# Performance work log

Measured on AMD Instinct MI355X. Metric: run time of the kernel, lower is better.

Reference implementation:

```python
import jax, jax.numpy as jnp
import numpy as np

ALPHA = 0.0005
TAU = 0.2


def setup_inputs() -> dict:
    key = jax.random.key(0)
    k1, k2, k3 = jax.random.split(key, 3)
    output = jax.random.normal(k1, (8192, 1000), dtype=jnp.float32)
    target = jax.random.normal(k2, (8192, 1000), dtype=jnp.float32)
    conv_w = jax.random.normal(k3, (256, 256, 128, 3), dtype=jnp.float32)
    return {"output": output, "target": target, "conv_w": conv_w}


def reference(output, target, conv_w):
    # base loss (nn.MSELoss with default 'mean' reduction)
    loss = jnp.mean((output - target) ** 2)

    # Diversity regularizer: pairwise cosine similarity between slices
    # conv_w[:, :, i, :] along dim 2 ('filters' = size(2) in the original).
    F = conv_w.shape[2]
    # V: [F, D] with D = out_ch * in_ch * kw
    V = jnp.transpose(conv_w, (2, 0, 1, 3)).reshape(F, -1)
    norms = jnp.linalg.norm(V, axis=1)                      # [F]
    G = (V @ V.T) / (norms[:, None] * norms[None, :])       # [F, F] cosine Gram

    # keep entries with tau < sim <= 1 and i != j
    offdiag = ~jnp.eye(F, dtype=bool)
    mask = (G > TAU) & (G <= 1.0) & offdiag
    reg = jnp.sum(jnp.where(mask, G, jnp.zeros((), dtype=G.dtype)))

    return loss + ALPHA * reg
```

## Files before the change

### kernel.cpp

```cpp
#include <hip/hip_runtime.h>
#include <hip/hip_bf16.h>


typedef __attribute__((ext_vector_type(8))) short bf16x8;
typedef __attribute__((ext_vector_type(4))) float f32x4;

#define ALPHA 0.0005f
#define TAU 0.2f

#define FDIM 128
#define NGRAM 1024
#define NMSE 2048
#define BLK_FLOATS 24576
#define NPAIRQ 8192
#define GRAM_ELEMS 16384
#define MSE_N4 2048000

__device__ __forceinline__ unsigned int pack_bf2(float lo, float hi) {
    union { float f; unsigned int u; } a, b;
    a.f = lo; b.f = hi;
    unsigned int al = (a.u + 0x7fffu + ((a.u >> 16) & 1u)) >> 16;
    unsigned int bh = (b.u + 0x7fffu + ((b.u >> 16) & 1u)) & 0xffff0000u;
    return (al & 0xffffu) | bh;
}

__device__ __forceinline__ uint4 make_frag(const float3& a, const float3& b) {
    uint4 r;
    r.x = pack_bf2(a.x, a.y);
    r.y = pack_bf2(a.z, b.x);
    r.z = pack_bf2(b.y, b.z);
    r.w = 0;
    return r;
}

__device__ __forceinline__ void load4(const float* __restrict__ p00,
                                      const float* __restrict__ p10,
                                      int c, float3 (&L)[4]) {
    const int co = c * 3072;
    L[0] = *reinterpret_cast<const float3*>(p00 + co);
    L[1] = *reinterpret_cast<const float3*>(p00 + co + 384);
    L[2] = *reinterpret_cast<const float3*>(p10 + co);
    L[3] = *reinterpret_cast<const float3*>(p10 + co + 384);
    __builtin_amdgcn_sched_barrier(0);
}

__device__ __forceinline__ void gram_chunk(
        const float* __restrict__ p00, const float* __restrict__ p10,
        int pre_c, bool dopre, float3 (&buf)[4],
        uint4 (*fragbuf)[64], int wave, int lane,
        f32x4 (&acc0)[8], f32x4 (&acc1)[8]) {
    const uint4 fA0 = make_frag(buf[0], buf[1]);
    const uint4 fA1 = make_frag(buf[2], buf[3]);
    if (dopre) load4(p00, p10, pre_c, buf);
    asm volatile("s_waitcnt lgkmcnt(0)" ::: "memory");
    __builtin_amdgcn_sched_barrier(0);
    __builtin_amdgcn_s_barrier();
    __builtin_amdgcn_sched_barrier(0);
    fragbuf[2 * wave][lane] = fA0;
    fragbuf[2 * wave + 1][lane] = fA1;
    asm volatile("s_waitcnt lgkmcnt(0)" ::: "memory");
    __builtin_amdgcn_sched_barrier(0);
    __builtin_amdgcn_s_barrier();
    __builtin_amdgcn_sched_barrier(0);
    const bf16x8 va0 = *reinterpret_cast<const bf16x8*>(&fA0);
    const bf16x8 va1 = *reinterpret_cast<const bf16x8*>(&fA1);
#pragma unroll
    for (int cc = 0; cc < 8; ++cc) {
        const uint4 fb = fragbuf[cc][lane];
        const bf16x8 vb = *reinterpret_cast<const bf16x8*>(&fb);
        acc0[cc] = __builtin_amdgcn_mfma_f32_16x16x32_bf16(va0, vb, acc0[cc], 0, 0, 0);
        acc1[cc] = __builtin_amdgcn_mfma_f32_16x16x32_bf16(va1, vb, acc1[cc], 0, 0, 0);
    }
}

__global__ void __launch_bounds__(256, 4) fused_kernel(
        const float* __restrict__ o, const float* __restrict__ t,
        const float* __restrict__ conv,
        float* __restrict__ mse_part, unsigned int* __restrict__ pp) {
    __shared__ uint4 fragbuf[8][64];
    __shared__ float red[4];
    const int tid = threadIdx.x;
    const int lane = tid & 63;
    const int wave = tid >> 6;

    if (blockIdx.x >= NGRAM) {
        const int mb = blockIdx.x - NGRAM;
        const int gid = mb * 256 + tid;
        const f32x4* o4 = reinterpret_cast<const f32x4*>(o);
        const f32x4* t4 = reinterpret_cast<const f32x4*>(t);
        float s = 0.f;
        for (int i = gid; i < MSE_N4; i += NMSE * 256) {
            f32x4 a = o4[i], b = t4[i];
            f32x4 d = a - b;
            s += d[0]*d[0] + d[1]*d[1] + d[2]*d[2] + d[3]*d[3];
        }
        for (int off = 32; off; off >>= 1) s += __shfl_down(s, off);
        if (lane == 0) red[wave] = s;
        __syncthreads();
        if (tid == 0) mse_part[mb] = red[0] + red[1] + red[2] + red[3];
        return;
    }

    const int g = lane >> 4;
    const int fl = lane & 15;
    const float* bp = conv + (size_t)blockIdx.x * BLK_FLOATS;
    const float* p00 = bp + (2 * g) * 384 + (32 * wave + fl) * 3;
    const float* p10 = p00 + 48;

    f32x4 acc0[8], acc1[8];
#pragma unroll
    for (int cc = 0; cc < 8; ++cc) { acc0[cc] = (f32x4)0.f; acc1[cc] = (f32x4)0.f; }

    float3 LA[4], LB[4];
    load4(p00, p10, 0, LA);
    load4(p00, p10, 1, LB);
#pragma unroll
    for (int c = 0; c < 8; c += 2) {
        gram_chunk(p00, p10, c + 2, c + 2 < 8, LA, fragbuf, wave, lane, acc0, acc1);
        gram_chunk(p00, p10, c + 3, c + 3 < 8, LB, fragbuf, wave, lane, acc0, acc1);
    }

    unsigned int* myp = pp + (size_t)blockIdx.x * NPAIRQ;
    const int colr = lane & 15;
    const int rsub = (lane >> 4) << 2;
#pragma unroll
    for (int cc = 0; cc < 8; ++cc) {
        const int col = cc * 16 + colr;
#pragma unroll
        for (int j = 0; j < 4; ++j) {
            const int pr = wave * 16 + rsub + j;
            myp[pr * FDIM + col] = pack_bf2(acc0[cc][j], acc1[cc][j]);
        }
    }
}

__global__ void __launch_bounds__(256) reduce_kernel(
        const unsigned int* __restrict__ pp, float* __restrict__ gram) {
    __shared__ float red[16][16][2];
    const int tid = threadIdx.x;
    const int u = tid & 15;
    const int s = tid >> 4;
    const int qq = blockIdx.x * 16 + u;
    float lo = 0.f, hi = 0.f;
#pragma unroll 8
    for (int b = s * 64; b < s * 64 + 64; ++b) {
        const unsigned int v = pp[(size_t)b * NPAIRQ + qq];
        lo += __uint_as_float(v << 16);
        hi += __uint_as_float(v & 0xffff0000u);
    }
    red[s][u][0] = lo; red[s][u][1] = hi;
    __syncthreads();
    if (tid < 32) {
        const int u2 = tid >> 1, h = tid & 1;
        float x = 0.f;
#pragma unroll
        for (int s2 = 0; s2 < 16; ++s2) x += red[s2][u2][h];
        gram[(blockIdx.x * 16 + u2) * 2 + h] = x;
    }
}

__global__ void __launch_bounds__(256) finalize_kernel(
        const float* __restrict__ gram, const float* __restrict__ mse_part,
        float* __restrict__ out) {
    __shared__ float rn[FDIM];
    __shared__ float redS[4], redM[4];
    const int tid = threadIdx.x;
    if (tid < FDIM) {
        const int row = tid;
        const int pr = (row >> 5) * 16 + (row & 15);
        const int h = (row >> 4) & 1;
        rn[row] = rsqrtf(gram[(pr * FDIM + row) * 2 + h]);
    }
    __syncthreads();
    float s = 0.f;
    for (int i = tid; i < GRAM_ELEMS; i += 256) {
        const int h = i & 1;
        const int qq = i >> 1;
        const int col = qq & 127;
        const int pr = qq >> 7;
        const int row = (pr >> 4) * 32 + (pr & 15) + (h << 4);
        const float gv = gram[i] * rn[row] * rn[col];
        if (row != col && gv > TAU && gv <= 1.0f) s += gv;
    }
    float m = 0.f;
#pragma unroll 8
    for (int j = 0; j < 8; ++j) m += mse_part[tid * 8 + j];
    for (int off = 32; off; off >>= 1) {
        s += __shfl_down(s, off);
        m += __shfl_down(m, off);
    }
    if ((tid & 63) == 0) { redS[tid >> 6] = s; redM[tid >> 6] = m; }
    __syncthreads();
    if (tid == 0)
        out[0] = (redM[0] + redM[1] + redM[2] + redM[3]) * (1.0f / 8192000.0f) +
                 ALPHA * (redS[0] + redS[1] + redS[2] + redS[3]);
}

extern "C" void kernel_launch(void* const* d_in, const int* in_sizes, int n_in,
                              void* d_out, int out_size, void* d_ws, size_t ws_size,
                              hipStream_t stream) {
    const float* output = (const float*)d_in[0];
    const float* target = (const float*)d_in[1];
    const float* conv   = (const float*)d_in[2];
    float* out = (float*)d_out;

    float* wsf       = (float*)d_ws;
    float* mse_part  = wsf;
    float* gram      = wsf + NMSE;
    unsigned int* pp = (unsigned int*)(wsf + NMSE + GRAM_ELEMS);
    (void)ws_size;

    fused_kernel<<<NGRAM + NMSE, 256, 0, stream>>>(output, target, conv,
                                                   mse_part, pp);
    reduce_kernel<<<NPAIRQ / 16, 256, 0, stream>>>(pp, gram);
    finalize_kernel<<<1, 256, 0, stream>>>(gram, mse_part, out);
}
```

Baseline: 64.22 us.

## Double-buffer Gram LDS fragments and interleave MSE blocks with Gram blocks

The LDS fragment buffer is now double-buffered, which removes one of the two block barriers per chunk: writes to the alternate buffer no longer have to wait for readers of the current one. Block indices are also remapped so every third block does Gram work and the other two do MSE. This mixes compute-heavy MFMA blocks with bandwidth-bound MSE blocks on each CU. It uses twice the LDS, and relies on the 1:2 ratio matching NGRAM:NMSE exactly.

```diff
diff --git a/kernel.cpp b/kernel.cpp
--- a/kernel.cpp
+++ b/kernel.cpp
@@ -46,18 +46,14 @@
 
 __device__ __forceinline__ void gram_chunk(
         const float* __restrict__ p00, const float* __restrict__ p10,
-        int pre_c, bool dopre, float3 (&buf)[4],
-        uint4 (*fragbuf)[64], int wave, int lane,
+        int pre_c, bool dopre, float3 (&buf)[4], int pb,
+        uint4 (*fragbuf)[8][64], int wave, int lane,
         f32x4 (&acc0)[8], f32x4 (&acc1)[8]) {
     const uint4 fA0 = make_frag(buf[0], buf[1]);
     const uint4 fA1 = make_frag(buf[2], buf[3]);
     if (dopre) load4(p00, p10, pre_c, buf);
-    asm volatile("s_waitcnt lgkmcnt(0)" ::: "memory");
-    __builtin_amdgcn_sched_barrier(0);
-    __builtin_amdgcn_s_barrier();
-    __builtin_amdgcn_sched_barrier(0);
-    fragbuf[2 * wave][lane] = fA0;
-    fragbuf[2 * wave + 1][lane] = fA1;
+    fragbuf[pb][2 * wave][lane] = fA0;
+    fragbuf[pb][2 * wave + 1][lane] = fA1;
     asm volatile("s_waitcnt lgkmcnt(0)" ::: "memory");
     __builtin_amdgcn_sched_barrier(0);
     __builtin_amdgcn_s_barrier();
@@ -66,7 +62,7 @@
     const bf16x8 va1 = *reinterpret_cast<const bf16x8*>(&fA1);
 #pragma unroll
     for (int cc = 0; cc < 8; ++cc) {
-        const uint4 fb = fragbuf[cc][lane];
+        const uint4 fb = fragbuf[pb][cc][lane];
         const bf16x8 vb = *reinterpret_cast<const bf16x8*>(&fb);
         acc0[cc] = __builtin_amdgcn_mfma_f32_16x16x32_bf16(va0, vb, acc0[cc], 0, 0, 0);
         acc1[cc] = __builtin_amdgcn_mfma_f32_16x16x32_bf16(va1, vb, acc1[cc], 0, 0, 0);
@@ -77,14 +73,16 @@
         const float* __restrict__ o, const float* __restrict__ t,
         const float* __restrict__ conv,
         float* __restrict__ mse_part, unsigned int* __restrict__ pp) {
-    __shared__ uint4 fragbuf[8][64];
+    __shared__ uint4 fragbuf[2][8][64];
     __shared__ float red[4];
     const int tid = threadIdx.x;
     const int lane = tid & 63;
     const int wave = tid >> 6;
-
-    if (blockIdx.x >= NGRAM) {
-        const int mb = blockIdx.x - NGRAM;
+    const int b3 = blockIdx.x / 3;
+    const int r3 = blockIdx.x - 3 * b3;
+
+    if (r3 != 0) {
+        const int mb = 2 * b3 + (r3 - 1);
         const int gid = mb * 256 + tid;
         const f32x4* o4 = reinterpret_cast<const f32x4*>(o);
         const f32x4* t4 = reinterpret_cast<const f32x4*>(t);
@@ -101,9 +99,10 @@
         return;
     }
 
+    const int gb = b3;
     const int g = lane >> 4;
     const int fl = lane & 15;
-    const float* bp = conv + (size_t)blockIdx.x * BLK_FLOATS;
+    const float* bp = conv + (size_t)gb * BLK_FLOATS;
     const float* p00 = bp + (2 * g) * 384 + (32 * wave + fl) * 3;
     const float* p10 = p00 + 48;
 
@@ -116,11 +115,11 @@
     load4(p00, p10, 1, LB);
 #pragma unroll
     for (int c = 0; c < 8; c += 2) {
-        gram_chunk(p00, p10, c + 2, c + 2 < 8, LA, fragbuf, wave, lane, acc0, acc1);
-        gram_chunk(p00, p10, c + 3, c + 3 < 8, LB, fragbuf, wave, lane, acc0, acc1);
-    }
-
-    unsigned int* myp = pp + (size_t)blockIdx.x * NPAIRQ;
+        gram_chunk(p00, p10, c + 2, c + 2 < 8, LA, 0, fragbuf, wave, lane, acc0, acc1);
+        gram_chunk(p00, p10, c + 3, c + 3 < 8, LB, 1, fragbuf, wave, lane, acc0, acc1);
+    }
+
+    unsigned int* myp = pp + (size_t)gb * NPAIRQ;
     const int colr = lane & 15;
     const int rsub = (lane >> 4) << 2;
 #pragma unroll
```

New measurement: 66.85 us. +4.1%, slower.
